# Kernel tuning notes

Measured on AMD Instinct MI355X. Metric: run time of the kernel, lower is better.

The kernel has to match this reference:

```python
import jax, jax.numpy as jnp
import numpy as np

THRESHOLD = 0.3

def ternary_ste(w, threshold=THRESHOLD):
    # hard threshold to {-1, 0, +1}; straight-through in bwd via stop_gradient trick
    q = jnp.where(w > threshold, 1.0, jnp.where(w < -threshold, -1.0, 0.0)).astype(w.dtype)
    return w + jax.lax.stop_gradient(q - w)

def setup_inputs() -> dict:
    key = jax.random.key(0)
    k1, k2 = jax.random.split(key)
    x = jax.random.normal(k1, (16, 4096, 512), dtype=jnp.float32)
    weight = jax.random.normal(k2, (512, 512), dtype=jnp.float32) * 0.1  # nn.Parameter(randn*0.1)
    return {"x": x, "weight": weight}

def reference(x, weight):
    qw = ternary_ste(weight)  # [out_dim, in_dim]
    # F.linear(x, W) == x @ W.T
    return jnp.einsum('bsi,oi->bso', x, qw)
```

## Files before the change

kernel.cpp:

```cpp
#include <hip/hip_runtime.h>


#define TH    0.3f
#define NSLOT 12
#define ROWS  16
#define KDIM  512
#define NDIM  512

__global__ __launch_bounds__(64) void build_tbl(const float* __restrict__ w,
                                                int* __restrict__ counts,
                                                int* __restrict__ tbl) {
    const int o    = blockIdx.x;
    const int lane = threadIdx.x;
    __shared__ int c;
    __shared__ int se[KDIM];
    if (lane == 0) c = 0;
    __syncthreads();
    const float* row = w + (size_t)o * KDIM;
    for (int i = lane; i < KDIM; i += 64) {
        float v = row[i];
        if (v > TH || v < -TH) {
            int pos = atomicAdd(&c, 1);
            se[pos] = (i << 1) | (v < 0.0f ? 1 : 0);
        }
    }
    __syncthreads();
    const int cnt = c;
    if (lane == 0) counts[o] = cnt;
    for (int k = lane; k < NSLOT; k += 64)
        tbl[o * NSLOT + k] = (k < cnt) ? se[k] : 0;
}

__global__ __launch_bounds__(512, 8) void ternary_mm(
        const float* __restrict__ x, const float* __restrict__ w,
        const int* __restrict__ counts, const int* __restrict__ tbl,
        float* __restrict__ out, int ntiles) {
    __shared__ float4 xs4[ROWS * KDIM / 4];
    float* xs = (float*)xs4;

    const int t   = threadIdx.x;
    const int cnt = counts[t];
    int e[NSLOT];
#pragma unroll
    for (int k = 0; k < NSLOT; ++k) e[k] = tbl[t * NSLOT + k];

    for (int tile = blockIdx.x; tile < ntiles; tile += gridDim.x) {
        const size_t base = (size_t)tile * ROWS * KDIM;

        __syncthreads();
        const float4* src = (const float4*)(x + base);
#pragma unroll
        for (int j = 0; j < (ROWS * KDIM / 4) / 512; ++j)
            xs4[j * 512 + t] = src[j * 512 + t];
        __syncthreads();

        if (cnt <= NSLOT) {
#pragma unroll
            for (int r = 0; r < ROWS; ++r) {
                float acc = 0.0f;
#pragma unroll
                for (int k = 0; k < NSLOT; ++k) {
                    if (k < cnt) {
                        int   ent = e[k];
                        float v   = xs[r * KDIM + (ent >> 1)];
                        acc += (ent & 1) ? -v : v;
                    }
                }
                out[base + (size_t)r * NDIM + t] = acc;
            }
        } else {
            const float* wrow = w + (size_t)t * KDIM;
            for (int r = 0; r < ROWS; ++r) {
                float acc = 0.0f;
                for (int i = 0; i < KDIM; ++i) {
                    float wv = wrow[i];
                    float v  = xs[r * KDIM + i];
                    acc += (wv > TH) ? v : ((wv < -TH) ? -v : 0.0f);
                }
                out[base + (size_t)r * NDIM + t] = acc;
            }
        }
    }
}

extern "C" void kernel_launch(void* const* d_in, const int* in_sizes, int n_in,
                              void* d_out, int out_size, void* d_ws, size_t ws_size,
                              hipStream_t stream) {
    const float* x = (const float*)d_in[0];
    const float* w = (const float*)d_in[1];
    float* out = (float*)d_out;

    int* counts = (int*)d_ws;
    int* tbl    = counts + NDIM;

    const int nrows  = in_sizes[0] / KDIM;
    const int ntiles = nrows / ROWS;

    build_tbl<<<NDIM, 64, 0, stream>>>(w, counts, tbl);
    ternary_mm<<<1024, 512, 0, stream>>>(x, w, counts, tbl, out, ntiles);
}
```

Measured before the change: 243.2 us.

## Sort output columns by nonzero count and stage outputs through shared memory

Adds a kernel that sorts output columns by their count of nonzero ternary weights so lanes in a wavefront have similar loop trip counts, with a wave-uniform max bound to cut divergence. NSLOT is raised to 16 so more columns take the sparse fast path. Each slot entry now serves 8 rows at once, and the sign is applied with an XOR instead of a select. Because of the permutation, results are written back into shared memory and stored to global as coalesced float4 writes. In exchange there is an extra kernel launch, extra barriers, and more registers per thread.

```diff
diff --git a/kernel.cpp b/kernel.cpp
--- a/kernel.cpp
+++ b/kernel.cpp
@@ -2,8 +2,9 @@
 
 
 #define TH    0.3f
-#define NSLOT 12
+#define NSLOT 16
 #define ROWS  16
+#define HALF  8
 #define KDIM  512
 #define NDIM  512
 
@@ -31,54 +32,118 @@
         tbl[o * NSLOT + k] = (k < cnt) ? se[k] : 0;
 }
 
+__global__ __launch_bounds__(512) void sort_cols(const int* __restrict__ counts,
+                                                 const int* __restrict__ tbl,
+                                                 int* __restrict__ perm,
+                                                 int* __restrict__ scnt,
+                                                 int* __restrict__ stbl) {
+    const int t = threadIdx.x;
+    const int cnt = counts[t];
+    const int key = cnt < (NSLOT + 1) ? cnt : (NSLOT + 1);
+    __shared__ int base[NSLOT + 2];
+    if (t < NSLOT + 2) base[t] = 0;
+    __syncthreads();
+    atomicAdd(&base[key], 1);
+    __syncthreads();
+    if (t == 0) {
+        int run = 0;
+        for (int c2 = NSLOT + 1; c2 >= 0; --c2) { int h = base[c2]; base[c2] = run; run += h; }
+    }
+    __syncthreads();
+    const int pos = atomicAdd(&base[key], 1);
+    perm[pos] = t;
+    scnt[pos] = cnt;
+#pragma unroll
+    for (int k = 0; k < NSLOT; ++k) stbl[pos * NSLOT + k] = tbl[t * NSLOT + k];
+}
+
 __global__ __launch_bounds__(512, 8) void ternary_mm(
         const float* __restrict__ x, const float* __restrict__ w,
-        const int* __restrict__ counts, const int* __restrict__ tbl,
-        float* __restrict__ out, int ntiles) {
-    __shared__ float4 xs4[ROWS * KDIM / 4];
-    float* xs = (float*)xs4;
+        const int* __restrict__ perm, const int* __restrict__ scnt,
+        const int* __restrict__ stbl, float* __restrict__ out, int ntiles) {
+    __shared__ float xs[ROWS * KDIM];
 
-    const int t   = threadIdx.x;
-    const int cnt = counts[t];
+    const int t  = threadIdx.x;
+    const int c  = perm[t];
+    const int ct = scnt[t];
     int e[NSLOT];
 #pragma unroll
-    for (int k = 0; k < NSLOT; ++k) e[k] = tbl[t * NSLOT + k];
+    for (int k = 0; k < NSLOT; ++k) e[k] = stbl[t * NSLOT + k];
+
+    const int fast = (ct <= NSLOT) ? ct : 0;
+    int wm = fast;
+#pragma unroll
+    for (int off = 32; off; off >>= 1) { int o2 = __shfl_xor(wm, off); wm = wm > o2 ? wm : o2; }
+    wm = __builtin_amdgcn_readfirstlane(wm);
 
     for (int tile = blockIdx.x; tile < ntiles; tile += gridDim.x) {
-        const size_t base = (size_t)tile * ROWS * KDIM;
+        const size_t base = (size_t)tile * (ROWS * KDIM);
 
         __syncthreads();
-        const float4* src = (const float4*)(x + base);
-#pragma unroll
-        for (int j = 0; j < (ROWS * KDIM / 4) / 512; ++j)
-            xs4[j * 512 + t] = src[j * 512 + t];
+        {
+            const float4* src = (const float4*)(x + base);
+            float4 st0 = src[0 * 512 + t];
+            float4 st1 = src[1 * 512 + t];
+            float4 st2 = src[2 * 512 + t];
+            float4 st3 = src[3 * 512 + t];
+            float4* dst = (float4*)xs;
+            dst[0 * 512 + t] = st0;
+            dst[1 * 512 + t] = st1;
+            dst[2 * 512 + t] = st2;
+            dst[3 * 512 + t] = st3;
+        }
         __syncthreads();
 
-        if (cnt <= NSLOT) {
 #pragma unroll
-            for (int r = 0; r < ROWS; ++r) {
-                float acc = 0.0f;
+        for (int h = 0; h < 2; ++h) {
+            float acc[HALF];
+#pragma unroll
+            for (int r = 0; r < HALF; ++r) acc[r] = 0.0f;
+
+            if (ct <= NSLOT) {
 #pragma unroll
                 for (int k = 0; k < NSLOT; ++k) {
-                    if (k < cnt) {
-                        int   ent = e[k];
-                        float v   = xs[r * KDIM + (ent >> 1)];
-                        acc += (ent & 1) ? -v : v;
+                    if (k >= wm) break;
+                    if (k < fast) {
+                        const int ent  = e[k];
+                        const int idx  = ent >> 1;
+                        const int smsk = (ent & 1) << 31;
+#pragma unroll
+                        for (int r = 0; r < HALF; ++r) {
+                            float v = xs[(h * HALF + r) * KDIM + idx];
+                            acc[r] += __int_as_float(__float_as_int(v) ^ smsk);
+                        }
                     }
                 }
-                out[base + (size_t)r * NDIM + t] = acc;
-            }
-        } else {
-            const float* wrow = w + (size_t)t * KDIM;
-            for (int r = 0; r < ROWS; ++r) {
-                float acc = 0.0f;
+            } else {
+                const float* wrow = w + (size_t)c * KDIM;
                 for (int i = 0; i < KDIM; ++i) {
                     float wv = wrow[i];
-                    float v  = xs[r * KDIM + i];
-                    acc += (wv > TH) ? v : ((wv < -TH) ? -v : 0.0f);
+                    if (wv > TH || wv < -TH) {
+                        const int smsk = (wv < 0.0f) ? (1 << 31) : 0;
+#pragma unroll
+                        for (int r = 0; r < HALF; ++r) {
+                            float v = xs[(h * HALF + r) * KDIM + i];
+                            acc[r] += __int_as_float(__float_as_int(v) ^ smsk);
+                        }
+                    }
                 }
-                out[base + (size_t)r * NDIM + t] = acc;
             }
+
+            __syncthreads();
+#pragma unroll
+            for (int r = 0; r < HALF; ++r)
+                xs[(h * HALF + r) * KDIM + c] = acc[r];
+        }
+        __syncthreads();
+
+        {
+            float4* dst = (float4*)(out + base);
+            const float4* s4 = (const float4*)xs;
+            dst[0 * 512 + t] = s4[0 * 512 + t];
+            dst[1 * 512 + t] = s4[1 * 512 + t];
+            dst[2 * 512 + t] = s4[2 * 512 + t];
+            dst[3 * 512 + t] = s4[3 * 512 + t];
         }
     }
 }
@@ -92,10 +157,14 @@
 
     int* counts = (int*)d_ws;
     int* tbl    = counts + NDIM;
+    int* perm   = tbl + NDIM * NSLOT;
+    int* scnt   = perm + NDIM;
+    int* stbl   = scnt + NDIM;
 
     const int nrows  = in_sizes[0] / KDIM;
     const int ntiles = nrows / ROWS;
 
     build_tbl<<<NDIM, 64, 0, stream>>>(w, counts, tbl);
-    ternary_mm<<<1024, 512, 0, stream>>>(x, w, counts, tbl, out, ntiles);
+    sort_cols<<<1, 512, 0, stream>>>(counts, tbl, perm, scnt, stbl);
+    ternary_mm<<<1024, 512, 0, stream>>>(x, w, perm, scnt, stbl, out, ntiles);
 }
```

Result: slower. 250.0 us (+2.8%).
